# Kernel tuning notes

Hardware: AMD Instinct MI355X
Metric: run time of the kernel (lower is better)

The kernel has to match this reference:

```python
import jax, jax.numpy as jnp
import numpy as np

V, E, H = 100000, 300, 256          # pretrained vectors, emb_dim, rep_dim
B, QLEN, DOC, S = 32, 32, 2048, 64  # batch, max_query_len, max_doc_len, max_num_sent
L = DOC // S                        # sentence length (lengths sum exactly to DOC)
VOCAB = V + 2                       # + extra token + padding idx


def _uniform(k, shape, scale):
    return jax.random.uniform(k, shape, jnp.float32, -scale, scale)


def setup_inputs() -> dict:
    key = jax.random.key(0)
    ks = jax.random.split(key, 16)
    s = 1.0 / np.sqrt(H)  # PyTorch GRU default init scale
    return {
        "queries": jax.random.randint(ks[0], (B, QLEN), 0, V),
        "query_lengths": jax.random.randint(ks[1], (B,), QLEN // 2, QLEN + 1).astype(jnp.int32),
        "docs": jax.random.randint(ks[2], (B, DOC), 0, V),
        "sentence_lengths": jnp.full((B, S), L, dtype=jnp.int32),
        "emb": jax.random.normal(ks[3], (VOCAB, E), jnp.float32) * 0.1,
        "q_wih": _uniform(ks[4], (3 * H, E), s), "q_whh": _uniform(ks[5], (3 * H, H), s),
        "q_bih": _uniform(ks[6], (3 * H,), s), "q_bhh": _uniform(ks[7], (3 * H,), s),
        "f_wih": _uniform(ks[8], (3 * H, E), s), "f_whh": _uniform(ks[9], (3 * H, H), s),
        "f_bih": _uniform(ks[10], (3 * H,), s), "f_bhh": _uniform(ks[11], (3 * H,), s),
        "b_wih": _uniform(ks[12], (3 * H, E), s), "b_whh": _uniform(ks[13], (3 * H, H), s),
        "b_bih": _uniform(ks[14], (3 * H,), s), "b_bhh": _uniform(ks[15], (3 * H,), s),
    }


def _gru(x, wih, whh, bih, bhh, reverse=False):
    # x: (B, T, E) -> hidden states (B, T, H); PyTorch GRU cell equations.
    xg = jnp.einsum('bte,ge->btg', x, wih) + bih  # (B, T, 3H) input projections

    def step(h, xt):
        gh = h @ whh.T + bhh
        ir, iz, inn = jnp.split(xt, 3, axis=-1)
        hr, hz, hn = jnp.split(gh, 3, axis=-1)
        r = jax.nn.sigmoid(ir + hr)
        z = jax.nn.sigmoid(iz + hz)
        n = jnp.tanh(inn + r * hn)
        hnew = (1.0 - z) * n + z * h
        return hnew, hnew

    h0 = jnp.zeros((x.shape[0], whh.shape[1]), x.dtype)
    _, hs = jax.lax.scan(step, h0, jnp.swapaxes(xg, 0, 1), reverse=reverse)
    return jnp.swapaxes(hs, 0, 1)


def reference(queries, query_lengths, docs, sentence_lengths, emb,
              q_wih, q_whh, q_bih, q_bhh,
              f_wih, f_whh, f_bih, f_bhh,
              b_wih, b_whh, b_bih, b_bhh):
    q_emb = emb[queries]  # (B, QLEN, E)
    d_emb = emb[docs]     # (B, DOC, E)

    # Ragged per-sentence mean pooling (_get_facts) as one segment-mean per doc.
    def seg_mean(xb, lens):
        ids = jnp.repeat(jnp.arange(S), lens, total_repeat_length=DOC)
        sums = jax.ops.segment_sum(xb, ids, num_segments=S)
        return sums / jnp.maximum(lens, 1)[:, None].astype(xb.dtype)

    facts = jax.vmap(seg_mean)(d_emb, sentence_lengths)  # (B, S, E)

    # Question GRU: hidden state at the last valid token (pack_padded semantics).
    q_hs = _gru(q_emb, q_wih, q_whh, q_bih, q_bhh)
    q_rep = q_hs[jnp.arange(B), query_lengths - 1][:, None, :]  # (B, 1, H)

    # Input fusion: bidirectional GRU over facts, fwd + bwd halves summed (dropout off / eval).
    f_out = (_gru(facts, f_wih, f_whh, f_bih, f_bhh)
             + _gru(facts, b_wih, b_whh, b_bih, b_bhh, reverse=True))  # (B, S, H)

    num_facts = jnp.sum(sentence_lengths > 0, axis=1)
    return q_rep, f_out, num_facts
```

## Files before the change

### kernel.cpp

```cpp
#include <hip/hip_runtime.h>

#define Bn   32
#define QL   32
#define DOCn 2048
#define Sn   64
#define En   300
#define Hn   256

typedef short bf16x8 __attribute__((ext_vector_type(8)));
typedef short s16x4  __attribute__((ext_vector_type(4)));
typedef float f32x4  __attribute__((ext_vector_type(4)));

static __device__ __forceinline__ float b2f(short s){
  unsigned int u = ((unsigned int)(unsigned short)s) << 16;
  float f; __builtin_memcpy(&f, &u, 4); return f;
}
static __device__ __forceinline__ short f2b(float f){
  unsigned int u; __builtin_memcpy(&u, &f, 4);
  u = u + 0x7fffu + ((u >> 16) & 1u);
  return (short)(u >> 16);
}
static __device__ __forceinline__ float sigm(float x){ return 1.0f/(1.0f+__expf(-x)); }
static __device__ __forceinline__ float tanhx(float x){ return 1.0f - 2.0f/(__expf(2.0f*x)+1.0f); }
static __device__ __forceinline__ f32x4 mfma16(bf16x8 a, bf16x8 b, f32x4 c){
  return __builtin_amdgcn_mfma_f32_16x16x32_bf16(a, b, c, 0, 0, 0);
}
static __device__ __forceinline__ void bar_lgkm(){
  asm volatile("s_waitcnt lgkmcnt(0)\n\ts_barrier" ::: "memory");
}

__global__ __launch_bounds__(256) void k_facts(
    const int* __restrict__ docs, const int* __restrict__ slens,
    const float* __restrict__ emb, short* __restrict__ facts)
{
  __shared__ int pref[2*Sn];
  const int blk = blockIdx.x;
  const int b = blk >> 6, s = blk & 63;
  const int tid = threadIdx.x;
  if (tid < Sn){
    const int v = slens[b*Sn + tid];
    int x = v;
#pragma unroll
    for (int d = 1; d < 64; d <<= 1){
      const int y = __shfl_up(x, d, 64);
      if (tid >= d) x += y;
    }
    pref[tid] = x - v;
    pref[Sn + tid] = v;
  }
  __syncthreads();
  const int off = pref[s];
  const int len = pref[Sn + s];
  const int e0 = tid;
  float a0 = 0.f, a1 = 0.f;
  const int* dtok = docs + b*DOCn + off;
  int tk = (len > 0) ? dtok[0] : 0;
  for (int l = 0; l < len; ++l){
    const int tkn = (l + 1 < len) ? dtok[l+1] : 0;
    const float* row = emb + (long)tk*En;
    a0 += row[e0];
    if (e0 + 256 < En) a1 += row[e0+256];
    tk = tkn;
  }
  const float inv = 1.0f / (float)(len > 0 ? len : 1);
  short* frow = facts + ((long)b*Sn + s)*En;
  frow[e0] = f2b(a0*inv);
  if (e0 + 256 < En) frow[e0+256] = f2b(a1*inv);
}

__global__ __launch_bounds__(256) void k_xg_q(
    const int* __restrict__ queries, const float* __restrict__ emb,
    const float* __restrict__ wih, const float* __restrict__ bih,
    short* __restrict__ xgi)
{
  __shared__ alignas(16) short Al[2][64][40];
  const int bm = blockIdx.x, bn = blockIdx.y;
  const int tid = threadIdx.x;
  const int l = tid & 63, w = tid >> 6;
  const int wm = w & 1, wn = w >> 1;
  const int l15 = l & 15, lq = l >> 4;

  bf16x8 bfr[2][10];
#pragma unroll
  for (int nt = 0; nt < 2; ++nt){
    const int g = bn*64 + wn*32 + nt*16 + l15;
    const float* wr = wih + (long)g*En;
#pragma unroll
    for (int kk = 0; kk < 10; ++kk){
      const int k0 = kk*32 + lq*8;
      bf16x8 v;
      if (k0 + 7 < En){
        const f32x4 f0 = *(const f32x4*)(wr + k0);
        const f32x4 f1 = *(const f32x4*)(wr + k0 + 4);
#pragma unroll
        for (int j = 0; j < 4; ++j){ v[j] = f2b(f0[j]); v[4+j] = f2b(f1[j]); }
      } else {
#pragma unroll
        for (int j = 0; j < 8; ++j){ const int k = k0 + j; v[j] = (k < En) ? f2b(wr[k]) : (short)0; }
      }
      bfr[nt][kk] = v;
    }
  }

  const int arow = l;
  const int ak8  = w*8;
  const int tok  = queries[bm*64 + arow];
  const float* asrc = emb + (long)tok*En;

  float ar[8];
#define LDA_Q(KK) do{ const int k0_ = (KK)*32 + ak8; \
    if (k0_ + 7 < En){ const f32x4 f0_ = *(const f32x4*)(asrc+k0_), f1_ = *(const f32x4*)(asrc+k0_+4); \
      ar[0]=f0_[0];ar[1]=f0_[1];ar[2]=f0_[2];ar[3]=f0_[3];ar[4]=f1_[0];ar[5]=f1_[1];ar[6]=f1_[2];ar[7]=f1_[3]; } \
    else { _Pragma("unroll") for (int j=0;j<8;++j){ const int k_=k0_+j; ar[j] = (k_<En)? asrc[k_] : 0.f; } } }while(0)
#define STA_Q(BUF) do{ s16x4 s0_ = (s16x4){f2b(ar[0]),f2b(ar[1]),f2b(ar[2]),f2b(ar[3])}; \
    s16x4 s1_ = (s16x4){f2b(ar[4]),f2b(ar[5]),f2b(ar[6]),f2b(ar[7])}; \
    *(s16x4*)&Al[BUF][arow][ak8] = s0_; *(s16x4*)&Al[BUF][arow][ak8+4] = s1_; }while(0)

  LDA_Q(0); STA_Q(0);
  __syncthreads();

  f32x4 acc[2][2] = {};
#pragma unroll
  for (int kk = 0; kk < 10; ++kk){
    if (kk < 9) LDA_Q(kk+1);
#pragma unroll
    for (int mt = 0; mt < 2; ++mt){
      bf16x8 a = *(const bf16x8*)&Al[kk&1][wm*32 + mt*16 + l15][lq*8];
      acc[mt][0] = mfma16(a, bfr[0][kk], acc[mt][0]);
      acc[mt][1] = mfma16(a, bfr[1][kk], acc[mt][1]);
    }
    if (kk < 9) STA_Q((kk+1)&1);
    __syncthreads();
  }
#undef LDA_Q
#undef STA_Q

#pragma unroll
  for (int nt = 0; nt < 2; ++nt){
    const int cg = bn*64 + wn*32 + nt*16 + l15;
    const float bias = bih[cg];
    const int gate = cg >> 8, hc = cg & 255;
#pragma unroll
    for (int mt = 0; mt < 2; ++mt){
      const int r0 = bm*64 + wm*32 + mt*16 + lq*4;
#pragma unroll
      for (int p = 0; p < 4; ++p){
        const int r = r0 + p;
        xgi[((long)((r & 31)*32 + (r >> 5)))*1024 + hc*4 + gate] = f2b(acc[mt][nt][p] + bias);
      }
    }
  }
}

__global__ __launch_bounds__(256) void k_xg_fb(
    const short* __restrict__ facts,
    const float* __restrict__ f_wih, const float* __restrict__ f_bih,
    const float* __restrict__ b_wih, const float* __restrict__ b_bih,
    short* __restrict__ f_xgi, short* __restrict__ b_xgi)
{
  __shared__ alignas(16) short Al[2][64][40];
  const float* wih = blockIdx.z ? b_wih : f_wih;
  const float* bih = blockIdx.z ? b_bih : f_bih;
  short*       xgi = blockIdx.z ? b_xgi : f_xgi;

  const int bm = blockIdx.x, bn = blockIdx.y;
  const int tid = threadIdx.x;
  const int l = tid & 63, w = tid >> 6;
  const int wm = w & 1, wn = w >> 1;
  const int l15 = l & 15, lq = l >> 4;

  bf16x8 bfr[2][10];
#pragma unroll
  for (int nt = 0; nt < 2; ++nt){
    const int g = bn*64 + wn*32 + nt*16 + l15;
    const float* wr = wih + (long)g*En;
#pragma unroll
    for (int kk = 0; kk < 10; ++kk){
      const int k0 = kk*32 + lq*8;
      bf16x8 v;
      if (k0 + 7 < En){
        const f32x4 f0 = *(const f32x4*)(wr + k0);
        const f32x4 f1 = *(const f32x4*)(wr + k0 + 4);
#pragma unroll
        for (int j = 0; j < 4; ++j){ v[j] = f2b(f0[j]); v[4+j] = f2b(f1[j]); }
      } else {
#pragma unroll
        for (int j = 0; j < 8; ++j){ const int k = k0 + j; v[j] = (k < En) ? f2b(wr[k]) : (short)0; }
      }
      bfr[nt][kk] = v;
    }
  }

  const int arow = l;
  const int ak8  = w*8;
  const short* asrc = facts + (long)(bm*64 + arow)*En;

  s16x4 a0_, a1_;
#define LDA_F(KK) do{ const int k0_ = (KK)*32 + ak8; \
    if (k0_ + 7 < En){ a0_ = *(const s16x4*)(asrc+k0_); a1_ = *(const s16x4*)(asrc+k0_+4); } \
    else { _Pragma("unroll") for (int j=0;j<4;++j){ const int ka_=k0_+j, kb_=k0_+4+j; \
      a0_[j] = (ka_<En)? asrc[ka_] : (short)0; a1_[j] = (kb_<En)? asrc[kb_] : (short)0; } } }while(0)
#define STA_F(BUF) do{ *(s16x4*)&Al[BUF][arow][ak8] = a0_; *(s16x4*)&Al[BUF][arow][ak8+4] = a1_; }while(0)

  LDA_F(0); STA_F(0);
  __syncthreads();

  f32x4 acc[2][2] = {};
#pragma unroll
  for (int kk = 0; kk < 10; ++kk){
    if (kk < 9) LDA_F(kk+1);
#pragma unroll
    for (int mt = 0; mt < 2; ++mt){
      bf16x8 a = *(const bf16x8*)&Al[kk&1][wm*32 + mt*16 + l15][lq*8];
      acc[mt][0] = mfma16(a, bfr[0][kk], acc[mt][0]);
      acc[mt][1] = mfma16(a, bfr[1][kk], acc[mt][1]);
    }
    if (kk < 9) STA_F((kk+1)&1);
    __syncthreads();
  }
#undef LDA_F
#undef STA_F

#pragma unroll
  for (int nt = 0; nt < 2; ++nt){
    const int cg = bn*64 + wn*32 + nt*16 + l15;
    const float bias = bih[cg];
    const int gate = cg >> 8, hc = cg & 255;
#pragma unroll
    for (int mt = 0; mt < 2; ++mt){
      const int r0 = bm*64 + wm*32 + mt*16 + lq*4;
#pragma unroll
      for (int p = 0; p < 4; ++p){
        const int r = r0 + p;
        xgi[((long)((r & 63)*32 + (r >> 6)))*1024 + hc*4 + gate] = f2b(acc[mt][nt][p] + bias);
      }
    }
  }
}

__global__ __launch_bounds__(1024) void k_gru(
    const short* __restrict__ q_xg, const short* __restrict__ f_xg,
    const short* __restrict__ b_xg,
    const float* __restrict__ q_whh, const float* __restrict__ q_bhh,
    const float* __restrict__ f_whh, const float* __restrict__ f_bhh,
    const float* __restrict__ b_whh, const float* __restrict__ b_bhh,
    const int* __restrict__ qlens,
    short* __restrict__ f_hs, short* __restrict__ b_hs,
    float* __restrict__ dout)
{
  __shared__ alignas(16) short hl[2*16*264];
  __shared__ alignas(16) short wl[7*1024*8];

  const int gru = blockIdx.x >> 1;
  const int mh  = blockIdx.x & 1;
  const int tid = threadIdx.x;
  const int l = tid & 63, w = tid >> 6;
  const int l15 = l & 15, lq = l >> 4;

  const float* whh = (gru == 0) ? q_whh : (gru == 1) ? f_whh : b_whh;
  const float* bhh = (gru == 0) ? q_bhh : (gru == 1) ? f_bhh : b_bhh;
  const short* xgp = (gru == 0) ? q_xg  : (gru == 1) ? f_xg  : b_xg;
  const int T = (gru == 0) ? QL : Sn;

  const int c = w*16 + l15;

  bf16x8 wf[3][6];
  float bias[3];
#pragma unroll
  for (int gi = 0; gi < 3; ++gi){
    const int g = gi*256 + c;
    const float* wr = whh + (long)g*Hn;
#pragma unroll
    for (int kk = 0; kk < 8; ++kk){
      const f32x4 f0 = *(const f32x4*)(wr + kk*32 + lq*8);
      const f32x4 f1 = *(const f32x4*)(wr + kk*32 + lq*8 + 4);
      bf16x8 v;
#pragma unroll
      for (int j = 0; j < 4; ++j){ v[j] = f2b(f0[j]); v[4+j] = f2b(f1[j]); }
      if (kk < 5 || (kk == 5 && gi < 2)) wf[gi][kk] = v;
      else if (kk == 5)                  *(bf16x8*)&wl[(6*1024 + tid)*8] = v;
      else                               *(bf16x8*)&wl[(((kk-6)*3 + gi)*1024 + tid)*8] = v;
    }
    bias[gi] = bhh[g];
  }

  float hreg[4] = {};
  int qlen_m[4];
#pragma unroll
  for (int p = 0; p < 4; ++p) qlen_m[p] = (gru == 0) ? qlens[mh*16 + lq*4 + p] : -1;

  const int vo  = (mh*16 + lq*4)*1024 + c*4;
  const int svo = (mh*16 + lq*4)*256 + c;
  short* hsp = (gru == 1) ? f_hs : b_hs;
  float* qdst = dout + (mh*16 + lq*4)*Hn + c;

  s16x4 preA[4], preB[4];

#define TOF(TT) ((gru == 2) ? (T - 1 - (TT)) : (TT))
#define LOADP(PRE, TI) do{ const short* sb_ = xgp + (long)(TI)*32768 + vo; \
    PRE[0] = *(const s16x4*)(sb_); \
    PRE[1] = *(const s16x4*)(sb_ + 1024); \
    PRE[2] = *(const s16x4*)(sb_ + 2048); \
    PRE[3] = *(const s16x4*)(sb_ + 3072); }while(0)

#define GRU_STEP(TT, DOM, HIN, HOUT, PRE) do{ \
    f32x4 acc0 = (f32x4){bias[0],bias[0],bias[0],bias[0]}; \
    f32x4 acc1 = (f32x4){bias[1],bias[1],bias[1],bias[1]}; \
    f32x4 acc2 = (f32x4){bias[2],bias[2],bias[2],bias[2]}; \
    if (DOM){ \
      _Pragma("unroll") for (int kk = 0; kk < 5; ++kk){ \
        const bf16x8 a = *(const bf16x8*)&(HIN)[l15*264 + kk*32 + lq*8]; \
        acc0 = mfma16(a, wf[0][kk], acc0); \
        acc1 = mfma16(a, wf[1][kk], acc1); \
        acc2 = mfma16(a, wf[2][kk], acc2); \
      } \
      { const bf16x8 a = *(const bf16x8*)&(HIN)[l15*264 + 5*32 + lq*8]; \
        const bf16x8 w2 = *(const bf16x8*)&wl[(6*1024 + tid)*8]; \
        acc0 = mfma16(a, wf[0][5], acc0); \
        acc1 = mfma16(a, wf[1][5], acc1); \
        acc2 = mfma16(a, w2, acc2); } \
      { const bf16x8 a = *(const bf16x8*)&(HIN)[l15*264 + 6*32 + lq*8]; \
        const bf16x8 w0 = *(const bf16x8*)&wl[(0*1024 + tid)*8]; \
        const bf16x8 w1 = *(const bf16x8*)&wl[(1*1024 + tid)*8]; \
        const bf16x8 w2 = *(const bf16x8*)&wl[(2*1024 + tid)*8]; \
        acc0 = mfma16(a, w0, acc0); \
        acc1 = mfma16(a, w1, acc1); \
        acc2 = mfma16(a, w2, acc2); } \
      { const bf16x8 a = *(const bf16x8*)&(HIN)[l15*264 + 7*32 + lq*8]; \
        const bf16x8 w0 = *(const bf16x8*)&wl[(3*1024 + tid)*8]; \
        const bf16x8 w1 = *(const bf16x8*)&wl[(4*1024 + tid)*8]; \
        const bf16x8 w2 = *(const bf16x8*)&wl[(5*1024 + tid)*8]; \
        acc0 = mfma16(a, w0, acc0); \
        acc1 = mfma16(a, w1, acc1); \
        acc2 = mfma16(a, w2, acc2); } \
    } \
    const int t_ = TOF(TT); \
    short* hst = hsp + (long)t_*8192 + svo; \
    _Pragma("unroll") for (int p = 0; p < 4; ++p){ \
      const float ir = b2f(PRE[p][0]), iz = b2f(PRE[p][1]), in_ = b2f(PRE[p][2]); \
      const float rr = sigm(ir + acc0[p]); \
      const float zz = sigm(iz + acc1[p]); \
      const float nn = tanhx(in_ + rr*acc2[p]); \
      const float hn = (1.0f - zz)*nn + zz*hreg[p]; \
      hreg[p] = hn; \
      (HOUT)[(lq*4 + p)*264 + c] = f2b(hn); \
      if (gru == 0){ if (t_ == qlen_m[p] - 1) qdst[p*Hn] = hn; } \
      else { hst[p*256] = f2b(hn); } \
    } \
  }while(0)

  short* h0 = hl;
  short* h1 = hl + 4224;

  LOADP(preA, TOF(0));
  LOADP(preB, TOF(1));
  __builtin_amdgcn_sched_barrier(0);
  GRU_STEP(0, 0, h1, h0, preA);
  bar_lgkm();
  LOADP(preA, TOF(2));
  __builtin_amdgcn_sched_barrier(0);
  GRU_STEP(1, 1, h0, h1, preB);
  bar_lgkm();

  for (int tt = 2; tt < T; tt += 2){
    const int tiB = (tt+1 < T) ? (tt+1) : (T-1);
    LOADP(preB, TOF(tiB));
    __builtin_amdgcn_sched_barrier(0);
    GRU_STEP(tt, 1, h1, h0, preA);
    bar_lgkm();
    const int tiA = (tt+2 < T) ? (tt+2) : (T-1);
    LOADP(preA, TOF(tiA));
    __builtin_amdgcn_sched_barrier(0);
    GRU_STEP(tt+1, 1, h0, h1, preB);
    bar_lgkm();
  }
#undef TOF
#undef LOADP
#undef GRU_STEP
}

__global__ __launch_bounds__(256) void k_combine(
    const short* __restrict__ f_hs, const short* __restrict__ b_hs,
    const int* __restrict__ slens, float* __restrict__ dout)
{
  const int i4 = (blockIdx.x*256 + threadIdx.x) * 4;
  const s16x4 fv = *(const s16x4*)(f_hs + i4);
  const s16x4 bv = *(const s16x4*)(b_hs + i4);
  const int t = i4 >> 13, bb = (i4 >> 8) & 31, cc = i4 & 255;
  f32x4 o;
#pragma unroll
  for (int j = 0; j < 4; ++j) o[j] = b2f(fv[j]) + b2f(bv[j]);
  *(f32x4*)(dout + Bn*Hn + ((long)bb << 14) + (t << 8) + cc) = o;
  if (blockIdx.x == 0 && threadIdx.x < Bn){
    const int* ls = slens + threadIdx.x*Sn;
    int cnt = 0;
#pragma unroll
    for (int s = 0; s < Sn; ++s) cnt += (ls[s] > 0) ? 1 : 0;
    dout[Bn*Hn + Bn*Sn*Hn + threadIdx.x] = (float)cnt;
  }
}

extern "C" void kernel_launch(void* const* d_in, const int* in_sizes, int n_in,
                              void* d_out, int out_size, void* d_ws, size_t ws_size,
                              hipStream_t stream)
{
  const int*   queries = (const int*)d_in[0];
  const int*   qlens   = (const int*)d_in[1];
  const int*   docs    = (const int*)d_in[2];
  const int*   slens   = (const int*)d_in[3];
  const float* emb     = (const float*)d_in[4];
  const float* q_wih   = (const float*)d_in[5];
  const float* q_whh   = (const float*)d_in[6];
  const float* q_bih   = (const float*)d_in[7];
  const float* q_bhh   = (const float*)d_in[8];
  const float* f_wih   = (const float*)d_in[9];
  const float* f_whh   = (const float*)d_in[10];
  const float* f_bih   = (const float*)d_in[11];
  const float* f_bhh   = (const float*)d_in[12];
  const float* b_wih   = (const float*)d_in[13];
  const float* b_whh   = (const float*)d_in[14];
  const float* b_bih   = (const float*)d_in[15];
  const float* b_bhh   = (const float*)d_in[16];

  char* wsb = (char*)d_ws;
  short* f_xgi = (short*)(wsb);
  short* b_xgi = (short*)(wsb +  4194304);
  short* q_xgi = (short*)(wsb +  8388608);
  short* facts = (short*)(wsb + 10485760);
  short* f_hs  = (short*)(wsb + 10485760);
  short* b_hs  = (short*)(wsb + 11714560);

  float* dout = (float*)d_out;

  k_facts<<<dim3(Bn*Sn), 256, 0, stream>>>(docs, slens, emb, facts);
  k_xg_q <<<dim3(16, 12), 256, 0, stream>>>(queries, emb, q_wih, q_bih, q_xgi);
  k_xg_fb<<<dim3(32, 12, 2), 256, 0, stream>>>(facts, f_wih, f_bih, b_wih, b_bih, f_xgi, b_xgi);
  k_gru  <<<dim3(6), 1024, 0, stream>>>(q_xgi, f_xgi, b_xgi, q_whh, q_bhh,
                                        f_whh, f_bhh, b_whh, b_bhh,
                                        qlens, f_hs, b_hs, dout);
  k_combine<<<dim3(512), 256, 0, stream>>>(f_hs, b_hs, slens, dout);
}
```

Measured before the change: 503.5 us.

## Halve GRU block to 512 threads with all recurrent weights in registers

```diff
diff --git a/kernel.cpp b/kernel.cpp
--- a/kernel.cpp
+++ b/kernel.cpp
@@ -71,7 +71,7 @@
 __global__ __launch_bounds__(256) void k_xg_q(
     const int* __restrict__ queries, const float* __restrict__ emb,
     const float* __restrict__ wih, const float* __restrict__ bih,
-    short* __restrict__ xgi)
+    const float* __restrict__ bhh, short* __restrict__ xgi)
 {
   __shared__ alignas(16) short Al[2][64][40];
   const int bm = blockIdx.x, bn = blockIdx.y;
@@ -138,7 +138,8 @@
 #pragma unroll
   for (int nt = 0; nt < 2; ++nt){
     const int cg = bn*64 + wn*32 + nt*16 + l15;
-    const float bias = bih[cg];
+    float bias = bih[cg];
+    if (cg < 512) bias += bhh[cg];
     const int gate = cg >> 8, hc = cg & 255;
 #pragma unroll
     for (int mt = 0; mt < 2; ++mt){
@@ -155,12 +156,15 @@
 __global__ __launch_bounds__(256) void k_xg_fb(
     const short* __restrict__ facts,
     const float* __restrict__ f_wih, const float* __restrict__ f_bih,
+    const float* __restrict__ f_bhh,
     const float* __restrict__ b_wih, const float* __restrict__ b_bih,
+    const float* __restrict__ b_bhh,
     short* __restrict__ f_xgi, short* __restrict__ b_xgi)
 {
   __shared__ alignas(16) short Al[2][64][40];
   const float* wih = blockIdx.z ? b_wih : f_wih;
   const float* bih = blockIdx.z ? b_bih : f_bih;
+  const float* bhh = blockIdx.z ? b_bhh : f_bhh;
   short*       xgi = blockIdx.z ? b_xgi : f_xgi;
 
   const int bm = blockIdx.x, bn = blockIdx.y;
@@ -224,7 +228,8 @@
 #pragma unroll
   for (int nt = 0; nt < 2; ++nt){
     const int cg = bn*64 + wn*32 + nt*16 + l15;
-    const float bias = bih[cg];
+    float bias = bih[cg];
+    if (cg < 512) bias += bhh[cg];
     const int gate = cg >> 8, hc = cg & 255;
 #pragma unroll
     for (int mt = 0; mt < 2; ++mt){
@@ -238,7 +243,7 @@
   }
 }
 
-__global__ __launch_bounds__(1024) void k_gru(
+__global__ __launch_bounds__(512, 2) void k_gru(
     const short* __restrict__ q_xg, const short* __restrict__ f_xg,
     const short* __restrict__ b_xg,
     const float* __restrict__ q_whh, const float* __restrict__ q_bhh,
@@ -249,7 +254,6 @@
     float* __restrict__ dout)
 {
   __shared__ alignas(16) short hl[2*16*264];
-  __shared__ alignas(16) short wl[7*1024*8];
 
   const int gru = blockIdx.x >> 1;
   const int mh  = blockIdx.x & 1;
@@ -262,120 +266,107 @@
   const short* xgp = (gru == 0) ? q_xg  : (gru == 1) ? f_xg  : b_xg;
   const int T = (gru == 0) ? QL : Sn;
 
-  const int c = w*16 + l15;
-
-  bf16x8 wf[3][6];
-  float bias[3];
+  const int cw = w*32 + l15;
+
+  bf16x8 wf[3][2][8];
+  float bhn[2];
 #pragma unroll
   for (int gi = 0; gi < 3; ++gi){
-    const int g = gi*256 + c;
-    const float* wr = whh + (long)g*Hn;
-#pragma unroll
-    for (int kk = 0; kk < 8; ++kk){
-      const f32x4 f0 = *(const f32x4*)(wr + kk*32 + lq*8);
-      const f32x4 f1 = *(const f32x4*)(wr + kk*32 + lq*8 + 4);
-      bf16x8 v;
-#pragma unroll
-      for (int j = 0; j < 4; ++j){ v[j] = f2b(f0[j]); v[4+j] = f2b(f1[j]); }
-      if (kk < 5 || (kk == 5 && gi < 2)) wf[gi][kk] = v;
-      else if (kk == 5)                  *(bf16x8*)&wl[(6*1024 + tid)*8] = v;
-      else                               *(bf16x8*)&wl[(((kk-6)*3 + gi)*1024 + tid)*8] = v;
-    }
-    bias[gi] = bhh[g];
-  }
-
-  float hreg[4] = {};
+#pragma unroll
+    for (int ct = 0; ct < 2; ++ct){
+      const int g = gi*256 + cw + ct*16;
+      const float* wr = whh + (long)g*Hn;
+#pragma unroll
+      for (int kk = 0; kk < 8; ++kk){
+        const f32x4 f0 = *(const f32x4*)(wr + kk*32 + lq*8);
+        const f32x4 f1 = *(const f32x4*)(wr + kk*32 + lq*8 + 4);
+        bf16x8 v;
+#pragma unroll
+        for (int j = 0; j < 4; ++j){ v[j] = f2b(f0[j]); v[4+j] = f2b(f1[j]); }
+        wf[gi][ct][kk] = v;
+      }
+      if (gi == 2) bhn[ct] = bhh[g];
+    }
+  }
+
+  float hreg[2][4] = {};
   int qlen_m[4];
 #pragma unroll
   for (int p = 0; p < 4; ++p) qlen_m[p] = (gru == 0) ? qlens[mh*16 + lq*4 + p] : -1;
 
-  const int vo  = (mh*16 + lq*4)*1024 + c*4;
-  const int svo = (mh*16 + lq*4)*256 + c;
+  const int row0 = mh*16 + lq*4;
+  const int vo  = row0*1024 + cw*4;
+  const int svo = row0*256 + cw;
   short* hsp = (gru == 1) ? f_hs : b_hs;
-  float* qdst = dout + (mh*16 + lq*4)*Hn + c;
-
-  s16x4 preA[4], preB[4];
+  float* qdst = dout + row0*Hn + cw;
+
+  s16x4 pre[2][4];
 
 #define TOF(TT) ((gru == 2) ? (T - 1 - (TT)) : (TT))
-#define LOADP(PRE, TI) do{ const short* sb_ = xgp + (long)(TI)*32768 + vo; \
-    PRE[0] = *(const s16x4*)(sb_); \
-    PRE[1] = *(const s16x4*)(sb_ + 1024); \
-    PRE[2] = *(const s16x4*)(sb_ + 2048); \
-    PRE[3] = *(const s16x4*)(sb_ + 3072); }while(0)
-
-#define GRU_STEP(TT, DOM, HIN, HOUT, PRE) do{ \
-    f32x4 acc0 = (f32x4){bias[0],bias[0],bias[0],bias[0]}; \
-    f32x4 acc1 = (f32x4){bias[1],bias[1],bias[1],bias[1]}; \
-    f32x4 acc2 = (f32x4){bias[2],bias[2],bias[2],bias[2]}; \
+#define LOADX(TI) do{ const short* sb_ = xgp + (long)(TI)*32768 + vo; \
+    _Pragma("unroll") for (int ct = 0; ct < 2; ++ct) \
+    _Pragma("unroll") for (int p = 0; p < 4; ++p) \
+      pre[ct][p] = *(const s16x4*)(sb_ + ct*64 + p*1024); }while(0)
+
+#define GRU_STEP(TT, DOM, HIN, HOUT) do{ \
+    f32x4 acc[3][2]; \
+    acc[0][0] = (f32x4){0.f,0.f,0.f,0.f}; acc[0][1] = (f32x4){0.f,0.f,0.f,0.f}; \
+    acc[1][0] = (f32x4){0.f,0.f,0.f,0.f}; acc[1][1] = (f32x4){0.f,0.f,0.f,0.f}; \
+    acc[2][0] = (f32x4){bhn[0],bhn[0],bhn[0],bhn[0]}; \
+    acc[2][1] = (f32x4){bhn[1],bhn[1],bhn[1],bhn[1]}; \
     if (DOM){ \
-      _Pragma("unroll") for (int kk = 0; kk < 5; ++kk){ \
+      _Pragma("unroll") for (int kk = 0; kk < 8; ++kk){ \
         const bf16x8 a = *(const bf16x8*)&(HIN)[l15*264 + kk*32 + lq*8]; \
-        acc0 = mfma16(a, wf[0][kk], acc0); \
-        acc1 = mfma16(a, wf[1][kk], acc1); \
-        acc2 = mfma16(a, wf[2][kk], acc2); \
+        _Pragma("unroll") for (int gi = 0; gi < 3; ++gi){ \
+          acc[gi][0] = mfma16(a, wf[gi][0][kk], acc[gi][0]); \
+          acc[gi][1] = mfma16(a, wf[gi][1][kk], acc[gi][1]); \
+        } \
       } \
-      { const bf16x8 a = *(const bf16x8*)&(HIN)[l15*264 + 5*32 + lq*8]; \
-        const bf16x8 w2 = *(const bf16x8*)&wl[(6*1024 + tid)*8]; \
-        acc0 = mfma16(a, wf[0][5], acc0); \
-        acc1 = mfma16(a, wf[1][5], acc1); \
-        acc2 = mfma16(a, w2, acc2); } \
-      { const bf16x8 a = *(const bf16x8*)&(HIN)[l15*264 + 6*32 + lq*8]; \
-        const bf16x8 w0 = *(const bf16x8*)&wl[(0*1024 + tid)*8]; \
-        const bf16x8 w1 = *(const bf16x8*)&wl[(1*1024 + tid)*8]; \
-        const bf16x8 w2 = *(const bf16x8*)&wl[(2*1024 + tid)*8]; \
-        acc0 = mfma16(a, w0, acc0); \
-        acc1 = mfma16(a, w1, acc1); \
-        acc2 = mfma16(a, w2, acc2); } \
-      { const bf16x8 a = *(const bf16x8*)&(HIN)[l15*264 + 7*32 + lq*8]; \
-        const bf16x8 w0 = *(const bf16x8*)&wl[(3*1024 + tid)*8]; \
-        const bf16x8 w1 = *(const bf16x8*)&wl[(4*1024 + tid)*8]; \
-        const bf16x8 w2 = *(const bf16x8*)&wl[(5*1024 + tid)*8]; \
-        acc0 = mfma16(a, w0, acc0); \
-        acc1 = mfma16(a, w1, acc1); \
-        acc2 = mfma16(a, w2, acc2); } \
     } \
     const int t_ = TOF(TT); \
     short* hst = hsp + (long)t_*8192 + svo; \
-    _Pragma("unroll") for (int p = 0; p < 4; ++p){ \
-      const float ir = b2f(PRE[p][0]), iz = b2f(PRE[p][1]), in_ = b2f(PRE[p][2]); \
-      const float rr = sigm(ir + acc0[p]); \
-      const float zz = sigm(iz + acc1[p]); \
-      const float nn = tanhx(in_ + rr*acc2[p]); \
-      const float hn = (1.0f - zz)*nn + zz*hreg[p]; \
-      hreg[p] = hn; \
-      (HOUT)[(lq*4 + p)*264 + c] = f2b(hn); \
-      if (gru == 0){ if (t_ == qlen_m[p] - 1) qdst[p*Hn] = hn; } \
-      else { hst[p*256] = f2b(hn); } \
+    _Pragma("unroll") for (int ct = 0; ct < 2; ++ct){ \
+      _Pragma("unroll") for (int p = 0; p < 4; ++p){ \
+        const float ir = b2f(pre[ct][p][0]), iz = b2f(pre[ct][p][1]), in_ = b2f(pre[ct][p][2]); \
+        const float rr = sigm(ir + acc[0][ct][p]); \
+        const float zz = sigm(iz + acc[1][ct][p]); \
+        const float nn = tanhx(in_ + rr*acc[2][ct][p]); \
+        const float hn = (1.0f - zz)*nn + zz*hreg[ct][p]; \
+        hreg[ct][p] = hn; \
+        (HOUT)[(lq*4 + p)*264 + cw + ct*16] = f2b(hn); \
+        if (gru == 0){ if (t_ == qlen_m[p] - 1) qdst[ct*16 + p*Hn] = hn; } \
+        else { hst[ct*16 + p*256] = f2b(hn); } \
+      } \
     } \
   }while(0)
 
   short* h0 = hl;
   short* h1 = hl + 4224;
 
-  LOADP(preA, TOF(0));
-  LOADP(preB, TOF(1));
-  __builtin_amdgcn_sched_barrier(0);
-  GRU_STEP(0, 0, h1, h0, preA);
+  LOADX(TOF(0));
+  GRU_STEP(0, 0, h1, h0);
+  LOADX(TOF(1));
   bar_lgkm();
-  LOADP(preA, TOF(2));
-  __builtin_amdgcn_sched_barrier(0);
-  GRU_STEP(1, 1, h0, h1, preB);
+  GRU_STEP(1, 1, h0, h1);
+  LOADX(TOF(2));
   bar_lgkm();
 
   for (int tt = 2; tt < T; tt += 2){
-    const int tiB = (tt+1 < T) ? (tt+1) : (T-1);
-    LOADP(preB, TOF(tiB));
-    __builtin_amdgcn_sched_barrier(0);
-    GRU_STEP(tt, 1, h1, h0, preA);
+    GRU_STEP(tt, 1, h1, h0);
+    {
+      const int ti = (tt+1 < T) ? (tt+1) : (T-1);
+      LOADX(TOF(ti));
+    }
     bar_lgkm();
-    const int tiA = (tt+2 < T) ? (tt+2) : (T-1);
-    LOADP(preA, TOF(tiA));
-    __builtin_amdgcn_sched_barrier(0);
-    GRU_STEP(tt+1, 1, h0, h1, preB);
+    GRU_STEP(tt+1, 1, h0, h1);
+    {
+      const int ti = (tt+2 < T) ? (tt+2) : (T-1);
+      LOADX(TOF(ti));
+    }
     bar_lgkm();
   }
 #undef TOF
-#undef LOADP
+#undef LOADX
 #undef GRU_STEP
 }
 
@@ -433,10 +424,11 @@
   float* dout = (float*)d_out;
 
   k_facts<<<dim3(Bn*Sn), 256, 0, stream>>>(docs, slens, emb, facts);
-  k_xg_q <<<dim3(16, 12), 256, 0, stream>>>(queries, emb, q_wih, q_bih, q_xgi);
-  k_xg_fb<<<dim3(32, 12, 2), 256, 0, stream>>>(facts, f_wih, f_bih, b_wih, b_bih, f_xgi, b_xgi);
-  k_gru  <<<dim3(6), 1024, 0, stream>>>(q_xgi, f_xgi, b_xgi, q_whh, q_bhh,
-                                        f_whh, f_bhh, b_whh, b_bhh,
-                                        qlens, f_hs, b_hs, dout);
+  k_xg_q <<<dim3(16, 12), 256, 0, stream>>>(queries, emb, q_wih, q_bih, q_bhh, q_xgi);
+  k_xg_fb<<<dim3(32, 12, 2), 256, 0, stream>>>(facts, f_wih, f_bih, f_bhh,
+                                               b_wih, b_bih, b_bhh, f_xgi, b_xgi);
+  k_gru  <<<dim3(6), 512, 0, stream>>>(q_xgi, f_xgi, b_xgi, q_whh, q_bhh,
+                                       f_whh, f_bhh, b_whh, b_bhh,
+                                       qlens, f_hs, b_hs, dout);
   k_combine<<<dim3(512), 256, 0, stream>>>(f_hs, b_hs, slens, dout);
 }
```

After: 586.4 us. +16.5%, slower.
